# Optimization experiments

Measured on AMD Instinct MI355X. Metric: run time of the kernel, lower is better.

## Reference

```python
import jax, jax.numpy as jnp
import numpy as np


def _l2norm(x, eps=1e-12):
    # F.normalize(dim=-1): x / max(||x||, eps)
    n = jnp.sqrt(jnp.sum(x * x, axis=-1, keepdims=True))
    return x / jnp.maximum(n, eps)


def setup_inputs() -> dict:
    key = jax.random.key(0)
    k1, k2, k3 = jax.random.split(key, 3)
    B, L, D = 4, 8192, 1024
    x = jax.random.normal(k1, (B, L, D), dtype=jnp.float32)
    # RoutingModule initializes q_proj/k_proj to identity; perturb slightly so the
    # projections are exercised but boundary probabilities stay realistic.
    Wq = jnp.eye(D, dtype=jnp.float32) + 0.02 * jax.random.normal(k2, (D, D), jnp.float32)
    Wk = jnp.eye(D, dtype=jnp.float32) + 0.02 * jax.random.normal(k3, (D, D), jnp.float32)
    return {"x": x, "Wq": Wq, "Wk": Wk, "chunk_divisor": 4}


def reference(x, Wq, Wk, chunk_divisor):
    B, L, D = x.shape
    max_chunks = L // chunk_divisor

    # ---- RoutingModule: p_t = 0.5*(1 - cos(q_t, k_{t-1})), p_0 = 1 ----
    q = _l2norm(jnp.einsum('bld,ed->ble', x[:, 1:], Wq))   # [B, L-1, D]
    k = _l2norm(jnp.einsum('bld,ed->ble', x[:, :-1], Wk))  # [B, L-1, D]
    cos_sim = jnp.einsum('bld,bld->bl', q, k)
    p = jnp.clip((1.0 - cos_sim) * 0.5, 0.0, 1.0)
    p = jnp.concatenate([jnp.ones((B, 1), p.dtype), p], axis=1)  # [B, L]
    boundary_mask = p >= 0.5

    # ---- ChunkLayer: gather boundary positions to the front, right-pad ----
    num_chunks = jnp.minimum(jnp.sum(boundary_mask, axis=-1), max_chunks)  # [B]
    token_idx = jnp.arange(L)[None, :] + (~boundary_mask).astype(jnp.int32) * L
    sorted_idx = jnp.argsort(token_idx, axis=1)
    take_idx = sorted_idx[:, :max_chunks]                                   # [B, C]
    chunked = jnp.take_along_axis(x, take_idx[:, :, None], axis=1)          # [B, C, D]
    pad_mask = jnp.arange(max_chunks)[None, :] < num_chunks[:, None]        # [B, C]
    chunked = chunked * pad_mask[:, :, None].astype(chunked.dtype)

    # ---- DeChunkLayer: EMA smoothing via associative scan, then scatter back ----
    C = max_chunks
    p_chunked = jnp.take_along_axis(p, take_idx, axis=1)
    p_chunked = jnp.clip(p_chunked, 1e-4, 1.0 - 1e-4)                       # [B, C]
    decay = jnp.broadcast_to((1.0 - p_chunked)[:, :, None], chunked.shape)  # [B, C, D]
    weighted_x = p_chunked[:, :, None] * chunked
    decay = decay.at[:, 0].set(0.0)
    weighted_x = weighted_x.at[:, 0].set(chunked[:, 0])

    def combine(left, right):
        d_l, v_l = left
        d_r, v_r = right
        return (d_l * d_r, v_r + d_r * v_l)

    _, smoothed = jax.lax.associative_scan(combine, (decay, weighted_x), axis=1)

    chunk_id = jnp.clip(jnp.cumsum(boundary_mask.astype(jnp.int32), axis=1) - 1, 0, C - 1)
    out = jnp.take_along_axis(smoothed, chunk_id[:, :, None], axis=1)       # [B, L, D]
    return out
```

## Files before the change

kernel.cpp:

```cpp
#include <hip/hip_runtime.h>
#include <math.h>

#define B_ 4
#define L_ 8192
#define D_ 1024
#define C_ 2048
#define CG 128
#define NG (C_/CG)
#define TAUF 3.0e-4f
#define MAXF 4096
#define FXF 4

typedef unsigned short ushortt;
using f32x4  = __attribute__((ext_vector_type(4))) float;
using bf16x8 = __attribute__((ext_vector_type(8))) short;

__device__ __forceinline__ ushortt f2bf(float f) {
    unsigned int u = __float_as_uint(f);
    u = (u + 0x7fffu + ((u >> 16) & 1u)) >> 16;
    return (ushortt)u;
}
__device__ __forceinline__ float bf2f(ushortt h) {
    return __uint_as_float(((unsigned int)h) << 16);
}

#define GLOAD16(gsrc, ldst) \
    __builtin_amdgcn_global_load_lds( \
        (const __attribute__((address_space(1))) unsigned int*)(gsrc), \
        (__attribute__((address_space(3))) unsigned int*)(ldst), 16, 0, 0)

__device__ __forceinline__ int swz32(int row, int g) { return g ^ ((row >> 1) & 3); }

__global__ __launch_bounds__(256) void k_prep(
    const float* __restrict__ Wq, const float* __restrict__ Wk,
    ushortt* __restrict__ eqb, ushortt* __restrict__ ekb)
{
    const float* W = blockIdx.y ? Wk : Wq;
    ushortt* E = blockIdx.y ? ekb : eqb;
    size_t i8 = ((size_t)blockIdx.x * 256 + threadIdx.x) * 8;
    int e = (int)(i8 >> 10), k0 = (int)(i8 & 1023);
    float4 a = *(const float4*)&W[i8];
    float4 b = *(const float4*)&W[i8 + 4];
    float v[8] = {a.x, a.y, a.z, a.w, b.x, b.y, b.z, b.w};
    ushortt o[8];
#pragma unroll
    for (int j = 0; j < 8; ++j) {
        float t = v[j] - ((k0 + j == e) ? 1.0f : 0.0f);
        o[j] = f2bf(t);
    }
    *(uint4*)&E[i8] = *(uint4*)o;
}

__global__ __launch_bounds__(256) void k_xb(
    const float* __restrict__ x, ushortt* __restrict__ xb)
{
    size_t i8 = ((size_t)blockIdx.x * 256 + threadIdx.x) * 8;
    float4 a = *(const float4*)&x[i8];
    float4 b = *(const float4*)&x[i8 + 4];
    float v[8] = {a.x, a.y, a.z, a.w, b.x, b.y, b.z, b.w};
    ushortt o[8];
#pragma unroll
    for (int j = 0; j < 8; ++j) o[j] = f2bf(v[j]);
    *(uint4*)&xb[i8] = *(uint4*)o;
}

__global__ __launch_bounds__(512, 4) void k_gemm(
    const ushortt* __restrict__ xb, const ushortt* __restrict__ eqb,
    const ushortt* __restrict__ ekb, float* __restrict__ partsg)
{
    __shared__ ushortt xsh[2][129 * 32];
    __shared__ ushortt eqsh[2][128 * 32];
    __shared__ ushortt eksh[2][128 * 32];
    __shared__ float part[128][2][3];

    const int tid = threadIdx.x;
    const int b = blockIdx.y;
    const int t0 = blockIdx.x * 128;
    const int z = blockIdx.z;
    const int lane = tid & 63;
    const int w = tid >> 6;
    const int wr = w >> 1;
    const int wc = w & 1;
    const int l15 = lane & 15, lg = lane >> 4;

    const int tq = tid & 255;
    const ushortt* egl = (tid < 256) ? eqb : ekb;

    float nq[8], nk[8], dt[8];
#pragma unroll
    for (int i = 0; i < 8; ++i) { nq[i] = 0.f; nk[i] = 0.f; dt[i] = 0.f; }

    f32x4 aqa[2][4], aka[2][4];
#pragma unroll
    for (int rb = 0; rb < 2; ++rb)
#pragma unroll
        for (int cf = 0; cf < 4; ++cf) {
            aqa[rb][cf] = (f32x4){0.f, 0.f, 0.f, 0.f};
            aka[rb][cf] = (f32x4){0.f, 0.f, 0.f, 0.f};
        }

    auto stage = [&](int it, int buf) {
        const int kb = it & 31, nb = it >> 5;
        const int k0 = kb * 32, e0 = z * 256 + nb * 128;
        uint4 extra;
        if (tid < 4)
            extra = *(const uint4*)&xb[((size_t)b * L_ + (t0 + 127)) * D_ + k0 + tid * 8];
        {
            int row = tid >> 2, g = tid & 3;
            int trow = t0 - 1 + row; if (trow < 0) trow = 0;
            const ushortt* src = &xb[((size_t)b * L_ + trow) * D_ + k0 + swz32(row, g) * 8];
            GLOAD16(src, &xsh[buf][tid * 8]);
        }
        ushortt* edst = (tid < 256) ? eqsh[buf] : eksh[buf];
#pragma unroll
        for (int r = 0; r < 2; ++r) {
            int row = r * 64 + (tq >> 2), g = tq & 3;
            const ushortt* src = &egl[(size_t)(e0 + row) * D_ + k0 + swz32(row, g) * 8];
            GLOAD16(src, &edst[r * 2048 + tq * 8]);
        }
        if (tid < 4)
            *(uint4*)&xsh[buf][128 * 32 + tid * 8] = extra;
    };

    stage(0, 0);
    __syncthreads();

    int buf = 0;
    for (int it = 0; it < 64; ++it) {
        if (it + 1 < 64) stage(it + 1, buf ^ 1);
        const ushortt* xsb = xsh[buf];
        const ushortt* eqs = eqsh[buf];
        const ushortt* eks = eksh[buf];
        {
            bf16x8 aq[2], ak[2];
#pragma unroll
            for (int rb = 0; rb < 2; ++rb) {
                int rq = 1 + wr * 32 + rb * 16 + l15;
                int rk = rq - 1;
                aq[rb] = *(const bf16x8*)&xsb[rq * 32 + swz32(rq, lg) * 8];
                ak[rb] = *(const bf16x8*)&xsb[rk * 32 + swz32(rk, lg) * 8];
            }
#pragma unroll
            for (int cf = 0; cf < 4; ++cf) {
                int er = wc * 64 + cf * 16 + l15;
                int off = er * 32 + swz32(er, lg) * 8;
                bf16x8 bq = *(const bf16x8*)&eqs[off];
#pragma unroll
                for (int rb = 0; rb < 2; ++rb)
                    aqa[rb][cf] = __builtin_amdgcn_mfma_f32_16x16x32_bf16(aq[rb], bq, aqa[rb][cf], 0, 0, 0);
                bf16x8 bk = *(const bf16x8*)&eks[off];
#pragma unroll
                for (int rb = 0; rb < 2; ++rb)
                    aka[rb][cf] = __builtin_amdgcn_mfma_f32_16x16x32_bf16(ak[rb], bk, aka[rb][cf], 0, 0, 0);
            }
        }
        if ((it & 31) == 31) {
            const int e0 = z * 256 + (it >> 5) * 128;
#pragma unroll
            for (int rb = 0; rb < 2; ++rb)
#pragma unroll
                for (int cf = 0; cf < 4; ++cf) {
                    const int ecol = e0 + wc * 64 + cf * 16 + l15;
                    const int tb = t0 + wr * 32 + rb * 16 + lg * 4;
                    const ushortt* xc = &xb[((size_t)b * L_ + tb) * D_ + ecol];
                    float xt0 = bf2f(xc[0]), xt1 = bf2f(xc[D_]);
                    float xt2 = bf2f(xc[2 * D_]), xt3 = bf2f(xc[3 * D_]);
                    float xm0 = (tb == 0) ? xt0 : bf2f(xc[-(int)D_]);
                    float xtv[4] = {xt0, xt1, xt2, xt3};
                    float xmv[4] = {xm0, xt0, xt1, xt2};
#pragma unroll
                    for (int r = 0; r < 4; ++r) {
                        float qe = xtv[r] + aqa[rb][cf][r];
                        float ke = xmv[r] + aka[rb][cf][r];
                        const int s = rb * 4 + r;
                        nq[s] = fmaf(qe, qe, nq[s]);
                        nk[s] = fmaf(ke, ke, nk[s]);
                        dt[s] = fmaf(qe, ke, dt[s]);
                    }
                }
#pragma unroll
            for (int rb = 0; rb < 2; ++rb)
#pragma unroll
                for (int cf = 0; cf < 4; ++cf) {
                    aqa[rb][cf] = (f32x4){0.f, 0.f, 0.f, 0.f};
                    aka[rb][cf] = (f32x4){0.f, 0.f, 0.f, 0.f};
                }
        }
        __syncthreads();
        buf ^= 1;
    }

#pragma unroll
    for (int m = 1; m < 16; m <<= 1) {
#pragma unroll
        for (int s = 0; s < 8; ++s) {
            nq[s] += __shfl_xor(nq[s], m);
            nk[s] += __shfl_xor(nk[s], m);
            dt[s] += __shfl_xor(dt[s], m);
        }
    }
    if (l15 == 0) {
#pragma unroll
        for (int s = 0; s < 8; ++s) {
            int rl = wr * 32 + (s >> 2) * 16 + lg * 4 + (s & 3);
            part[rl][wc][0] = nq[s];
            part[rl][wc][1] = nk[s];
            part[rl][wc][2] = dt[s];
        }
    }
    __syncthreads();
    if (tid < 128) {
        int t = t0 + tid;
        size_t o = ((size_t)(b * L_ + t) * 4 + z) * 3;
        partsg[o + 0] = part[tid][0][0] + part[tid][1][0];
        partsg[o + 1] = part[tid][0][1] + part[tid][1][1];
        partsg[o + 2] = part[tid][0][2] + part[tid][1][2];
    }
}

__global__ __launch_bounds__(256) void k_pfinal(
    const float* __restrict__ partsg, float* __restrict__ p,
    int* __restrict__ cnt, int* __restrict__ flags)
{
    int gid = blockIdx.x * 256 + threadIdx.x;
    int t = gid & (L_ - 1);
    const float4* pg = (const float4*)&partsg[(size_t)gid * 12];
    float4 v0 = pg[0], v1 = pg[1], v2 = pg[2];
    float a = v0.x + v0.w + v1.z + v2.y;
    float c = v0.y + v1.x + v1.w + v2.z;
    float d = v0.z + v1.y + v2.x + v2.w;
    float qn = fmaxf(sqrtf(a), 1e-12f);
    float kn = fmaxf(sqrtf(c), 1e-12f);
    float cs = d / (qn * kn);
    float pv = fminf(fmaxf((1.0f - cs) * 0.5f, 0.0f), 1.0f);
    if (t == 0) pv = 1.0f;
    p[gid] = pv;
    if (t > 0 && fabsf(cs) < TAUF) {
        int idx = atomicAdd(cnt, 1);
        if (idx < MAXF) flags[idx] = gid;
    }
}

__global__ __launch_bounds__(256) void k_fix(
    const float* __restrict__ x, const float* __restrict__ Wq,
    const float* __restrict__ Wk, const int* __restrict__ cnt,
    const int* __restrict__ flags, float* __restrict__ parts)
{
    int n = *cnt; if (n > MAXF) n = MAXF;
    const int m0 = blockIdx.x * FXF;
    if (m0 >= n) return;
    const int e0 = blockIdx.y * 128;

    __shared__ float xs[FXF * 2][1024];
    __shared__ float ws[2][128 * 17];
    __shared__ float comb[FXF * 4][128];
    __shared__ float red2[2][FXF][3];

    const int tid = threadIdx.x;
    const int e = tid & 127;
    const int kh = tid >> 7;

    {
        int row = tid >> 5, c0 = (tid & 31) * 32;
        int f = row >> 1, wh = row & 1;
        int sl = m0 + f;
        int gf = flags[(sl < n) ? sl : m0];
        int fb = gf >> 13, ft = (gf & (L_ - 1)) - wh;
        const float* src = &x[((size_t)fb * L_ + ft) * D_ + c0];
#pragma unroll
        for (int i = 0; i < 8; ++i)
            *(float4*)&xs[row][c0 + i * 4] = *(const float4*)&src[i * 4];
    }

    const int sr = tid >> 1, sk = (tid & 1) * 8;
    const float* gWq = &Wq[(size_t)(e0 + sr) * D_ + sk];
    const float* gWk = &Wk[(size_t)(e0 + sr) * D_ + sk];

    float acc[FXF][2];
#pragma unroll
    for (int f = 0; f < FXF; ++f) { acc[f][0] = 0.f; acc[f][1] = 0.f; }

    float4 pq0 = ((const float4*)gWq)[0], pq1 = ((const float4*)gWq)[1];
    float4 pk0 = ((const float4*)gWk)[0], pk1 = ((const float4*)gWk)[1];

    for (int kc = 0; kc < 64; ++kc) {
        __syncthreads();
        {
            int o = sr * 17 + sk;
            ws[0][o + 0] = pq0.x; ws[0][o + 1] = pq0.y; ws[0][o + 2] = pq0.z; ws[0][o + 3] = pq0.w;
            ws[0][o + 4] = pq1.x; ws[0][o + 5] = pq1.y; ws[0][o + 6] = pq1.z; ws[0][o + 7] = pq1.w;
            ws[1][o + 0] = pk0.x; ws[1][o + 1] = pk0.y; ws[1][o + 2] = pk0.z; ws[1][o + 3] = pk0.w;
            ws[1][o + 4] = pk1.x; ws[1][o + 5] = pk1.y; ws[1][o + 6] = pk1.z; ws[1][o + 7] = pk1.w;
        }
        if (kc + 1 < 64) {
            const float* nq2 = gWq + (kc + 1) * 16;
            const float* nk2 = gWk + (kc + 1) * 16;
            pq0 = ((const float4*)nq2)[0]; pq1 = ((const float4*)nq2)[1];
            pk0 = ((const float4*)nk2)[0]; pk1 = ((const float4*)nk2)[1];
        }
        __syncthreads();
        float wq[8], wk[8];
#pragma unroll
        for (int j = 0; j < 8; ++j) {
            wq[j] = ws[0][e * 17 + kh * 8 + j];
            wk[j] = ws[1][e * 17 + kh * 8 + j];
        }
        const int kbase = kc * 16 + kh * 8;
#pragma unroll
        for (int f = 0; f < FXF; ++f) {
            float aq = acc[f][0], ak = acc[f][1];
#pragma unroll
            for (int j2 = 0; j2 < 2; ++j2) {
                float4 xq = *(const float4*)&xs[f * 2][kbase + j2 * 4];
                float4 xk = *(const float4*)&xs[f * 2 + 1][kbase + j2 * 4];
                aq = fmaf(xq.x, wq[j2 * 4 + 0], aq); aq = fmaf(xq.y, wq[j2 * 4 + 1], aq);
                aq = fmaf(xq.z, wq[j2 * 4 + 2], aq); aq = fmaf(xq.w, wq[j2 * 4 + 3], aq);
                ak = fmaf(xk.x, wk[j2 * 4 + 0], ak); ak = fmaf(xk.y, wk[j2 * 4 + 1], ak);
                ak = fmaf(xk.z, wk[j2 * 4 + 2], ak); ak = fmaf(xk.w, wk[j2 * 4 + 3], ak);
            }
            acc[f][0] = aq; acc[f][1] = ak;
        }
    }

    __syncthreads();
#pragma unroll
    for (int f = 0; f < FXF; ++f) {
        comb[(f * 2 + 0) * 2 + kh][e] = acc[f][0];
        comb[(f * 2 + 1) * 2 + kh][e] = acc[f][1];
    }
    __syncthreads();
    if (tid < 128) {
        float r0[FXF], r1[FXF], r2[FXF];
#pragma unroll
        for (int f = 0; f < FXF; ++f) {
            float q = comb[(f * 2 + 0) * 2 + 0][e] + comb[(f * 2 + 0) * 2 + 1][e];
            float k = comb[(f * 2 + 1) * 2 + 0][e] + comb[(f * 2 + 1) * 2 + 1][e];
            r0[f] = q * q; r1[f] = k * k; r2[f] = q * k;
        }
#pragma unroll
        for (int m = 1; m < 64; m <<= 1) {
#pragma unroll
            for (int f = 0; f < FXF; ++f) {
                r0[f] += __shfl_xor(r0[f], m);
                r1[f] += __shfl_xor(r1[f], m);
                r2[f] += __shfl_xor(r2[f], m);
            }
        }
        if ((tid & 63) == 0) {
            int wv = tid >> 6;
#pragma unroll
            for (int f = 0; f < FXF; ++f) {
                red2[wv][f][0] = r0[f]; red2[wv][f][1] = r1[f]; red2[wv][f][2] = r2[f];
            }
        }
    }
    __syncthreads();
    if (tid < FXF) {
        float A  = red2[0][tid][0] + red2[1][tid][0];
        float Cc = red2[0][tid][1] + red2[1][tid][1];
        float Dd = red2[0][tid][2] + red2[1][tid][2];
        if (m0 + tid < n) {
            size_t o = ((size_t)(m0 + tid) * 8 + blockIdx.y) * 3;
            parts[o] = A; parts[o + 1] = Cc; parts[o + 2] = Dd;
        }
    }
}

__global__ __launch_bounds__(256) void k_fix_final(
    const int* __restrict__ cnt, const int* __restrict__ flags,
    const float* __restrict__ parts, float* __restrict__ p)
{
    int n = *cnt; if (n > MAXF) n = MAXF;
    int f = blockIdx.x * 256 + threadIdx.x;
    if (f >= n) return;
    float a = 0.f, c = 0.f, d = 0.f;
#pragma unroll
    for (int e = 0; e < 8; ++e) {
        size_t o = ((size_t)f * 8 + e) * 3;
        a += parts[o + 0]; c += parts[o + 1]; d += parts[o + 2];
    }
    float qn = fmaxf(sqrtf(a), 1e-12f);
    float kn = fmaxf(sqrtf(c), 1e-12f);
    float cs = d / (qn * kn);
    float pv = fminf(fmaxf((1.0f - cs) * 0.5f, 0.0f), 1.0f);
    p[flags[f]] = pv;
}

__global__ __launch_bounds__(1024) void k_boundaries(
    const float* __restrict__ p, int* __restrict__ take, int* __restrict__ nch,
    float2* __restrict__ cw, int* __restrict__ segev)
{
    const int b = blockIdx.x;
    const int tid = threadIdx.x;
    __shared__ int ssum[1024];
    __shared__ int tl[C_];

    float4 p0 = *(const float4*)&p[b * L_ + tid * 8];
    float4 p1 = *(const float4*)&p[b * L_ + tid * 8 + 4];
    float pv8[8] = {p0.x, p0.y, p0.z, p0.w, p1.x, p1.y, p1.z, p1.w};
    bool m[8];
    int local = 0;
#pragma unroll
    for (int j = 0; j < 8; ++j) {
        m[j] = (pv8[j] >= 0.5f);
        local += m[j] ? 1 : 0;
    }
    ssum[tid] = local;
    __syncthreads();
    for (int off = 1; off < 1024; off <<= 1) {
        int add = (tid >= off) ? ssum[tid - off] : 0;
        __syncthreads();
        ssum[tid] += add;
        __syncthreads();
    }
    const int total = ssum[1023];
    int rank = ssum[tid] - local;
#pragma unroll
    for (int j = 0; j < 8; ++j) {
        if (m[j]) {
            if (rank < C_) { take[b * C_ + rank] = tid * 8 + j; tl[rank] = tid * 8 + j; }
            ++rank;
        }
    }
    const int K = (total < C_) ? total : C_;
    if (tid == 0) nch[b] = K;
    for (int c = total + tid; c < C_; c += 1024) { take[b * C_ + c] = 0; tl[c] = 0; }
    __syncthreads();
    for (int c = tid; c < C_; c += 1024) {
        int idx = tl[c];
        float pc = p[b * L_ + idx];
        pc = fminf(fmaxf(pc, 1e-4f), 1.f - 1e-4f);
        float dc = (c == 0) ? 0.f : (1.f - pc);
        float wv = (c == 0) ? 1.f : pc;
        cw[b * C_ + c] = make_float2(dc, wv);
        segev[b * C_ + c] = (c + 1 < K) ? tl[c + 1] : L_;
    }
}

__global__ __launch_bounds__(256) void k_scan_local(
    const float* __restrict__ x, const int* __restrict__ take,
    const float2* __restrict__ cw, float* __restrict__ E, float* __restrict__ M)
{
    const int g = blockIdx.x, b = blockIdx.y, zq = blockIdx.z;
    const int d = zq * 256 + threadIdx.x;
    const int base = b * C_ + g * CG;

    float s = 0.f, mm = 1.f;
    for (int cc = 0; cc < CG; cc += 4) {
        int4 i4 = *(const int4*)&take[base + cc];
        float2 w0 = cw[base + cc], w1 = cw[base + cc + 1];
        float2 w2 = cw[base + cc + 2], w3 = cw[base + cc + 3];
        float x0 = x[((size_t)b * L_ + i4.x) * D_ + d];
        float x1 = x[((size_t)b * L_ + i4.y) * D_ + d];
        float x2 = x[((size_t)b * L_ + i4.z) * D_ + d];
        float x3 = x[((size_t)b * L_ + i4.w) * D_ + d];
        s = fmaf(w0.x, s, w0.y * x0); mm *= w0.x;
        s = fmaf(w1.x, s, w1.y * x1); mm *= w1.x;
        s = fmaf(w2.x, s, w2.y * x2); mm *= w2.x;
        s = fmaf(w3.x, s, w3.y * x3); mm *= w3.x;
    }
    E[((size_t)b * NG + g) * D_ + d] = s;
    if (threadIdx.x == 0 && zq == 0) M[b * NG + g] = mm;
}

__global__ __launch_bounds__(256) void k_scan_groups(
    const float* __restrict__ E, const float* __restrict__ M, float* __restrict__ carry)
{
    const int gid = blockIdx.x * 256 + threadIdx.x;
    const int b = gid >> 10, d = gid & 1023;
    float s = 0.f;
    for (int g = 0; g < NG; ++g) {
        carry[((size_t)b * NG + g) * D_ + d] = s;
        s = E[((size_t)b * NG + g) * D_ + d] + M[b * NG + g] * s;
    }
}

__global__ __launch_bounds__(256) void k_scan_out(
    const float* __restrict__ x, const int* __restrict__ take,
    const float2* __restrict__ cw, const int* __restrict__ segev,
    const int* __restrict__ nch, const float* __restrict__ carry,
    float* __restrict__ last_s, float* __restrict__ out)
{
    const int g = blockIdx.x, b = blockIdx.y, zq = blockIdx.z;
    const int d = zq * 256 + threadIdx.x;
    const int K = nch[b];
    const int c0 = g * CG;
    if (c0 >= K) return;
    const int c1 = (c0 + CG < K) ? (c0 + CG) : K;
    const int base = b * C_;

    float s = carry[((size_t)b * NG + g) * D_ + d];
    int idx = take[base + c0];
    float2 w0 = cw[base + c0];
    float xv = x[((size_t)b * L_ + idx) * D_ + d];
    for (int c = c0; c < c1; ++c) {
        int idxn = 0; float2 wn = make_float2(0.f, 0.f); float xn = 0.f;
        if (c + 1 < c1) {
            idxn = take[base + c + 1];
            wn = cw[base + c + 1];
            xn = x[((size_t)b * L_ + idxn) * D_ + d];
        }
        s = fmaf(w0.x, s, w0.y * xv);
        if (c == K - 1) {
            last_s[b * D_ + d] = s;
        } else {
            int sege = segev[base + c];
            for (int l = idx; l < sege; ++l)
                out[((size_t)b * L_ + l) * D_ + d] = s;
        }
        idx = idxn; w0 = wn; xv = xn;
    }
}

__global__ __launch_bounds__(256) void k_tail(
    const int* __restrict__ take, const int* __restrict__ nch,
    const float* __restrict__ last_s, float* __restrict__ out)
{
    const int b = blockIdx.y;
    const int tt0 = blockIdx.x * 8;
    const int K = nch[b];
    const int start = take[b * C_ + K - 1];
    if (tt0 + 8 <= start) return;
    float4 v = *(const float4*)&last_s[b * D_ + threadIdx.x * 4];
#pragma unroll
    for (int j = 0; j < 8; ++j) {
        int t = tt0 + j;
        if (t >= start)
            *(float4*)&out[((size_t)b * L_ + t) * D_ + threadIdx.x * 4] = v;
    }
}

extern "C" void kernel_launch(void* const* d_in, const int* in_sizes, int n_in,
                              void* d_out, int out_size, void* d_ws, size_t ws_size,
                              hipStream_t stream)
{
    (void)in_sizes; (void)n_in; (void)out_size;
    const float* x  = (const float*)d_in[0];
    const float* Wq = (const float*)d_in[1];
    const float* Wk = (const float*)d_in[2];
    float* out = (float*)d_out;

    char* ws = (char*)d_ws;
    float*  p      = (float*)(ws + 0);
    int*    take   = (int*)  (ws + 131072);
    int*    nch    = (int*)  (ws + 163840);
    float*  M      = (float*)(ws + 164096);
    float2* cw     = (float2*)(ws + 164608);
    int*    segev  = (int*)  (ws + 230144);
    float*  last_s = (float*)(ws + 262912);
    int*    cnt    = (int*)  (ws + 279296);
    int*    flags  = (int*)  (ws + 279552);
    float*  parts  = (float*)(ws + 295936);
    float*  E      = (float*)(ws + 689152);
    float*  carry  = (float*)(ws + 951296);
    ushortt* eqb   = (ushortt*)(ws + 1213440);
    ushortt* ekb   = (ushortt*)(ws + 3310592);
    if (ws_size < 5407744u) return;

    ushortt* xb = (ushortt*)d_out;
    float* partsg = (float*)((char*)d_out + 67108864);

    hipMemsetAsync(cnt, 0, 256, stream);
    k_prep<<<dim3(512, 2), 256, 0, stream>>>(Wq, Wk, eqb, ekb);
    k_xb<<<16384, 256, 0, stream>>>(x, xb);
    k_gemm<<<dim3(64, B_, 4), 512, 0, stream>>>(xb, eqb, ekb, partsg);
    k_pfinal<<<(B_ * L_) / 256, 256, 0, stream>>>(partsg, p, cnt, flags);
    k_fix<<<dim3(MAXF / FXF, 8), 256, 0, stream>>>(x, Wq, Wk, cnt, flags, parts);
    k_fix_final<<<MAXF / 256, 256, 0, stream>>>(cnt, flags, parts, p);
    k_boundaries<<<B_, 1024, 0, stream>>>(p, take, nch, cw, segev);
    dim3 g3(NG, B_, 4);
    k_scan_local<<<g3, 256, 0, stream>>>(x, take, cw, E, M);
    k_scan_groups<<<(B_ * D_) / 256, 256, 0, stream>>>(E, M, carry);
    k_scan_out<<<g3, 256, 0, stream>>>(x, take, cw, segev, nch, carry, last_s, out);
    k_tail<<<dim3(L_ / 8, B_), 256, 0, stream>>>(take, nch, last_s, out);
}
```

Measured before the change: 401.9 us.

## Retile GEMM to 64-wide E tiles with K=64 stages and 8 z-splits

Restructures the fused q/k projection GEMM so each block covers 128 output columns (two 64-column sub-tiles) instead of 256, with a K step of 64 per stage and an 8-way grid split over E. The LDS swizzle changes to an XOR over 8 groups for the wider rows. The partial-sum buffer doubles to 8 partials per token, and the finalisation kernel is updated to match. The aim is more blocks for occupancy and fewer barriers per unit of work, at the cost of reloading x tiles twice as often across z and more partial-sum traffic.

```diff
diff --git a/kernel.cpp b/kernel.cpp
--- a/kernel.cpp
+++ b/kernel.cpp
@@ -29,8 +29,6 @@
         (const __attribute__((address_space(1))) unsigned int*)(gsrc), \
         (__attribute__((address_space(3))) unsigned int*)(ldst), 16, 0, 0)
 
-__device__ __forceinline__ int swz32(int row, int g) { return g ^ ((row >> 1) & 3); }
-
 __global__ __launch_bounds__(256) void k_prep(
     const float* __restrict__ Wq, const float* __restrict__ Wk,
     ushortt* __restrict__ eqb, ushortt* __restrict__ ekb)
@@ -68,9 +66,9 @@
     const ushortt* __restrict__ xb, const ushortt* __restrict__ eqb,
     const ushortt* __restrict__ ekb, float* __restrict__ partsg)
 {
-    __shared__ ushortt xsh[2][129 * 32];
-    __shared__ ushortt eqsh[2][128 * 32];
-    __shared__ ushortt eksh[2][128 * 32];
+    __shared__ ushortt xsh[2][129 * 64];
+    __shared__ ushortt eqsh[2][64 * 64];
+    __shared__ ushortt eksh[2][64 * 64];
     __shared__ float part[128][2][3];
 
     const int tid = threadIdx.x;
@@ -90,60 +88,63 @@
 #pragma unroll
     for (int i = 0; i < 8; ++i) { nq[i] = 0.f; nk[i] = 0.f; dt[i] = 0.f; }
 
-    f32x4 aqa[2][4], aka[2][4];
+    f32x4 aqa[2][2], aka[2][2];
 #pragma unroll
     for (int rb = 0; rb < 2; ++rb)
 #pragma unroll
-        for (int cf = 0; cf < 4; ++cf) {
+        for (int cf = 0; cf < 2; ++cf) {
             aqa[rb][cf] = (f32x4){0.f, 0.f, 0.f, 0.f};
             aka[rb][cf] = (f32x4){0.f, 0.f, 0.f, 0.f};
         }
 
     auto stage = [&](int it, int buf) {
-        const int kb = it & 31, nb = it >> 5;
-        const int k0 = kb * 32, e0 = z * 256 + nb * 128;
+        const int kb = it & 15, nb = it >> 4;
+        const int k0 = kb * 64, e0 = z * 128 + nb * 64;
         uint4 extra;
-        if (tid < 4)
+        if (tid < 8)
             extra = *(const uint4*)&xb[((size_t)b * L_ + (t0 + 127)) * D_ + k0 + tid * 8];
-        {
-            int row = tid >> 2, g = tid & 3;
+#pragma unroll
+        for (int r = 0; r < 2; ++r) {
+            int row = r * 64 + (tid >> 3), kg = tid & 7;
             int trow = t0 - 1 + row; if (trow < 0) trow = 0;
-            const ushortt* src = &xb[((size_t)b * L_ + trow) * D_ + k0 + swz32(row, g) * 8];
-            GLOAD16(src, &xsh[buf][tid * 8]);
+            const ushortt* src = &xb[((size_t)b * L_ + trow) * D_ + k0 + ((kg ^ (row & 7)) << 3)];
+            GLOAD16(src, &xsh[buf][r * 4096 + tid * 8]);
         }
         ushortt* edst = (tid < 256) ? eqsh[buf] : eksh[buf];
 #pragma unroll
         for (int r = 0; r < 2; ++r) {
-            int row = r * 64 + (tq >> 2), g = tq & 3;
-            const ushortt* src = &egl[(size_t)(e0 + row) * D_ + k0 + swz32(row, g) * 8];
+            int row = r * 32 + (tq >> 3), kg = tq & 7;
+            const ushortt* src = &egl[(size_t)(e0 + row) * D_ + k0 + ((kg ^ (row & 7)) << 3)];
             GLOAD16(src, &edst[r * 2048 + tq * 8]);
         }
-        if (tid < 4)
-            *(uint4*)&xsh[buf][128 * 32 + tid * 8] = extra;
+        if (tid < 8)
+            *(uint4*)&xsh[buf][128 * 64 + tid * 8] = extra;
     };
 
     stage(0, 0);
     __syncthreads();
 
     int buf = 0;
-    for (int it = 0; it < 64; ++it) {
-        if (it + 1 < 64) stage(it + 1, buf ^ 1);
+    for (int it = 0; it < 32; ++it) {
+        if (it + 1 < 32) stage(it + 1, buf ^ 1);
         const ushortt* xsb = xsh[buf];
         const ushortt* eqs = eqsh[buf];
         const ushortt* eks = eksh[buf];
-        {
+#pragma unroll
+        for (int ks = 0; ks < 2; ++ks) {
+            const int kk = ks * 32 + lg * 8;
             bf16x8 aq[2], ak[2];
 #pragma unroll
             for (int rb = 0; rb < 2; ++rb) {
                 int rq = 1 + wr * 32 + rb * 16 + l15;
                 int rk = rq - 1;
-                aq[rb] = *(const bf16x8*)&xsb[rq * 32 + swz32(rq, lg) * 8];
-                ak[rb] = *(const bf16x8*)&xsb[rk * 32 + swz32(rk, lg) * 8];
+                aq[rb] = *(const bf16x8*)&xsb[rq * 64 + (kk ^ ((rq & 7) << 3))];
+                ak[rb] = *(const bf16x8*)&xsb[rk * 64 + (kk ^ ((rk & 7) << 3))];
             }
 #pragma unroll
-            for (int cf = 0; cf < 4; ++cf) {
-                int er = wc * 64 + cf * 16 + l15;
-                int off = er * 32 + swz32(er, lg) * 8;
+            for (int cf = 0; cf < 2; ++cf) {
+                int er = wc * 32 + cf * 16 + l15;
+                int off = er * 64 + (kk ^ ((er & 7) << 3));
                 bf16x8 bq = *(const bf16x8*)&eqs[off];
 #pragma unroll
                 for (int rb = 0; rb < 2; ++rb)
@@ -154,13 +155,13 @@
                     aka[rb][cf] = __builtin_amdgcn_mfma_f32_16x16x32_bf16(ak[rb], bk, aka[rb][cf], 0, 0, 0);
             }
         }
-        if ((it & 31) == 31) {
-            const int e0 = z * 256 + (it >> 5) * 128;
+        if ((it & 15) == 15) {
+            const int e0 = z * 128 + (it >> 4) * 64;
 #pragma unroll
             for (int rb = 0; rb < 2; ++rb)
 #pragma unroll
-                for (int cf = 0; cf < 4; ++cf) {
-                    const int ecol = e0 + wc * 64 + cf * 16 + l15;
+                for (int cf = 0; cf < 2; ++cf) {
+                    const int ecol = e0 + wc * 32 + cf * 16 + l15;
                     const int tb = t0 + wr * 32 + rb * 16 + lg * 4;
                     const ushortt* xc = &xb[((size_t)b * L_ + tb) * D_ + ecol];
                     float xt0 = bf2f(xc[0]), xt1 = bf2f(xc[D_]);
@@ -181,7 +182,7 @@
 #pragma unroll
             for (int rb = 0; rb < 2; ++rb)
 #pragma unroll
-                for (int cf = 0; cf < 4; ++cf) {
+                for (int cf = 0; cf < 2; ++cf) {
                     aqa[rb][cf] = (f32x4){0.f, 0.f, 0.f, 0.f};
                     aka[rb][cf] = (f32x4){0.f, 0.f, 0.f, 0.f};
                 }
@@ -211,7 +212,7 @@
     __syncthreads();
     if (tid < 128) {
         int t = t0 + tid;
-        size_t o = ((size_t)(b * L_ + t) * 4 + z) * 3;
+        size_t o = ((size_t)(b * L_ + t) * 8 + z) * 3;
         partsg[o + 0] = part[tid][0][0] + part[tid][1][0];
         partsg[o + 1] = part[tid][0][1] + part[tid][1][1];
         partsg[o + 2] = part[tid][0][2] + part[tid][1][2];
@@ -224,11 +225,12 @@
 {
     int gid = blockIdx.x * 256 + threadIdx.x;
     int t = gid & (L_ - 1);
-    const float4* pg = (const float4*)&partsg[(size_t)gid * 12];
+    const float4* pg = (const float4*)&partsg[(size_t)gid * 24];
     float4 v0 = pg[0], v1 = pg[1], v2 = pg[2];
-    float a = v0.x + v0.w + v1.z + v2.y;
-    float c = v0.y + v1.x + v1.w + v2.z;
-    float d = v0.z + v1.y + v2.x + v2.w;
+    float4 v3 = pg[3], v4 = pg[4], v5 = pg[5];
+    float a = v0.x + v0.w + v1.z + v2.y + v3.x + v3.w + v4.z + v5.y;
+    float c = v0.y + v1.x + v1.w + v2.z + v3.y + v4.x + v4.w + v5.z;
+    float d = v0.z + v1.y + v2.x + v2.w + v3.z + v4.y + v5.x + v5.w;
     float qn = fmaxf(sqrtf(a), 1e-12f);
     float kn = fmaxf(sqrtf(c), 1e-12f);
     float cs = d / (qn * kn);
@@ -563,7 +565,7 @@
     hipMemsetAsync(cnt, 0, 256, stream);
     k_prep<<<dim3(512, 2), 256, 0, stream>>>(Wq, Wk, eqb, ekb);
     k_xb<<<16384, 256, 0, stream>>>(x, xb);
-    k_gemm<<<dim3(64, B_, 4), 512, 0, stream>>>(xb, eqb, ekb, partsg);
+    k_gemm<<<dim3(64, B_, 8), 512, 0, stream>>>(xb, eqb, ekb, partsg);
     k_pfinal<<<(B_ * L_) / 256, 256, 0, stream>>>(partsg, p, cnt, flags);
     k_fix<<<dim3(MAXF / FXF, 8), 256, 0, stream>>>(x, Wq, Wk, cnt, flags, parts);
     k_fix_final<<<MAXF / 256, 256, 0, stream>>>(cnt, flags, parts, p);
```

After: 410.3 us. +2.1%, slower.
